# Kernel optimization log

Hardware: AMD Instinct MI355X
Metric: run time of the kernel (lower is better)

The kernel has to match this reference:

```python
import jax, jax.numpy as jnp
import numpy as np
from jax import lax

N_NODES = 64; N_GROUPS = 16; GROUP_SIZE = 4
B = 256; L = 64; CNN_C = 32; GH = 128; DH = 128; OUT = 64
E1 = 262144; E2 = 32768
GROUP_NODES = jnp.arange(N_NODES).reshape(N_GROUPS, GROUP_SIZE)

PARAM_SHAPES = [
    ('conv_w3', (N_NODES, CNN_C, 3)), ('conv_b3', (N_NODES, CNN_C)),
    ('conv_w5', (N_NODES, CNN_C, 5)), ('conv_b5', (N_NODES, CNN_C)),
    ('conv_w7', (N_NODES, CNN_C, 7)), ('conv_b7', (N_NODES, CNN_C)),
    ('tconv_w3', (N_NODES, CNN_C, 3)), ('tconv_b3', (N_NODES, CNN_C)),
    ('tconv_w5', (N_NODES, CNN_C, 5)), ('tconv_b5', (N_NODES, CNN_C)),
    ('tconv_w7', (N_NODES, CNN_C, 7)), ('tconv_b7', (N_NODES, CNN_C)),
    ('ff_w', (N_NODES, 6 * CNN_C, GH)), ('ff_b', (N_NODES, GH)),
    ('lower_w', (GH, GH)), ('lower_b', (GH,)),
    ('upper_w', (GH, GH)), ('upper_b', (GH,)),
    ('agg_w', (N_GROUPS, GROUP_SIZE * GH, GH)), ('agg_b', (N_GROUPS, GH)),
    ('disc_w', (N_GROUPS, 2 * GH, DH)), ('disc_b', (N_GROUPS, DH)),
    ('fc_w', (N_GROUPS * DH, OUT)), ('fc_b', (OUT,)),
]


def setup_inputs() -> dict:
    key = jax.random.key(0)
    ks = jax.random.split(key, 6 + len(PARAM_SHAPES))
    d = {
        'x1': jax.random.normal(ks[0], (B * N_NODES, 4, L), jnp.float32),
        'x2': jax.random.normal(ks[1], (B * N_NODES, 4, L), jnp.float32),
        'edge_index1': jax.random.randint(ks[2], (2, E1), 0, B * N_NODES),
        'edge_index2': jax.random.randint(ks[3], (2, E1), 0, B * N_NODES),
        'group_edge_index1': jax.random.randint(ks[4], (2, E2), 0, B * N_GROUPS),
        'group_edge_index2': jax.random.randint(ks[5], (2, E2), 0, B * N_GROUPS),
    }
    for i, (name, shape) in enumerate(PARAM_SHAPES):
        d[name] = jax.random.normal(ks[6 + i], shape, jnp.float32) * 0.05
    return d


def _grouped_conv_max(x, w, b, pad):
    # x: [B, N, Lx] (one input channel per node), w: [N, C, k], b: [N, C]
    N, C, k = w.shape
    y = lax.conv_general_dilated(x, w.reshape(N * C, 1, k), (1,), [(pad, pad)],
                                 feature_group_count=N,
                                 dimension_numbers=('NCH', 'OIH', 'NCH'))
    y = y + b.reshape(1, N * C, 1)
    return y.max(axis=2).reshape(x.shape[0], N, C)  # max over time per channel


def _gcn(x, edge_index, W, bias):
    # PyG GCNConv: add self loops, symmetric D^-1/2 (A+I) D^-1/2 normalization
    n = x.shape[0]
    loops = jnp.arange(n)
    src = jnp.concatenate([edge_index[0], loops])
    dst = jnp.concatenate([edge_index[1], loops])
    deg = jax.ops.segment_sum(jnp.ones(src.shape[0], x.dtype), dst, n)
    dinv = jnp.where(deg > 0, lax.rsqrt(deg), 0.0)
    h = x @ W
    msg = h[src] * (dinv[src] * dinv[dst])[:, None]
    return jax.ops.segment_sum(msg, dst, n) + bias


def reference(x1, x2, edge_index1, edge_index2, group_edge_index1, group_edge_index2,
              conv_w3, conv_b3, conv_w5, conv_b5, conv_w7, conv_b7,
              tconv_w3, tconv_b3, tconv_w5, tconv_b5, tconv_w7, tconv_b7,
              ff_w, ff_b, lower_w, lower_b, upper_w, upper_b,
              agg_w, agg_b, disc_w, disc_b, fc_w, fc_b):
    def encode(x, ei, gei):
        xr = x.reshape(B, N_NODES, 4, L)  # row = b*N_NODES + n -> x[n::N] == xr[:, n]
        feats = jnp.concatenate([
            _grouped_conv_max(xr[:, :, 0, :], conv_w3, conv_b3, 1),
            _grouped_conv_max(xr[:, :, 0, :], conv_w5, conv_b5, 2),
            _grouped_conv_max(xr[:, :, 0, :], conv_w7, conv_b7, 3),
            _grouped_conv_max(xr[:, :, 1, :-2], tconv_w3, tconv_b3, 1),
            _grouped_conv_max(xr[:, :, 2, :-4], tconv_w5, tconv_b5, 2),
            _grouped_conv_max(xr[:, :, 3, :-6], tconv_w7, tconv_b7, 3),
        ], axis=2)  # [B, N, 6C]
        feats = jax.nn.relu(feats)
        h = jax.nn.relu(jnp.einsum('bnf,nfh->bnh', feats, ff_w) + ff_b)  # per-node Linear
        h = _gcn(h.reshape(B * N_NODES, GH), ei, lower_w, lower_b)
        hg = h.reshape(B, N_NODES, GH)[:, GROUP_NODES]  # [B, G, S, GH]
        hg = hg.reshape(B, N_GROUPS, GROUP_SIZE * GH)
        hg = jnp.einsum('bgf,gfh->bgh', hg, agg_w) + agg_b  # per-group aggregate Linear
        hg = _gcn(hg.reshape(B * N_GROUPS, GH), gei, upper_w, upper_b)
        return jax.nn.relu(hg).reshape(B, N_GROUPS, GH)

    h1 = encode(x1, edge_index1, group_edge_index1)
    h2 = encode(x2, edge_index2, group_edge_index2)
    d = jnp.concatenate([h1, h2], axis=2)  # [B, G, 2*GH]
    d = jax.nn.relu(jnp.einsum('bgf,gfd->bgd', d, disc_w) + disc_b)  # per-group disc fc
    return d.reshape(B, N_GROUPS * DH) @ fc_w + fc_b  # [B, OUT]
```

## Files before the change

### kernel.cpp

```cpp
#include <hip/hip_runtime.h>
#include <hip/hip_bf16.h>

namespace {

constexpr int Bn      = 256;
constexpr int NNODES  = 64;
constexpr int NGROUPS = 16;
constexpr int L       = 64;
constexpr int C       = 32;
constexpr int GH      = 128;
constexpr int E1      = 262144;
constexpr int E2      = 32768;
constexpr int NROWS   = Bn * NNODES;
constexpr int GROWS   = Bn * NGROUPS;
constexpr int XROW    = 296;

template<int K, int LX>
__device__ __forceinline__ void convmax2(const float* __restrict__ xin_al,
                                         const float* __restrict__ wpa,
                                         const float* __restrict__ wpb,
                                         float& ma, float& mb)
{
    constexpr int PAD = (K - 1) / 2;
    constexpr int OFF = 3 - PAD;
    float wa[K], wb[K];
    #pragma unroll
    for (int i = 0; i < K; ++i) { wa[i] = wpa[i]; wb[i] = wpb[i]; }
    ma = -3.0e38f; mb = -3.0e38f;
    #pragma unroll
    for (int p0 = 0; p0 < LX; p0 += 16) {
        float xw[24];
        #pragma unroll
        for (int q = 0; q < 6; ++q) {
            const float4 v = *(const float4*)(xin_al + p0 + q * 4);
            xw[q * 4 + 0] = v.x; xw[q * 4 + 1] = v.y;
            xw[q * 4 + 2] = v.z; xw[q * 4 + 3] = v.w;
        }
        #pragma unroll
        for (int p = 0; p < 16; p += 2) {
            if (p0 + p + 1 < LX) {
                float sa0 = 0.f, sb0 = 0.f, sa1 = 0.f, sb1 = 0.f;
                #pragma unroll
                for (int i = 0; i < K; ++i) {
                    const float xv0 = xw[p + OFF + i];
                    const float xv1 = xw[p + 1 + OFF + i];
                    sa0 = fmaf(wa[i], xv0, sa0);
                    sb0 = fmaf(wb[i], xv0, sb0);
                    sa1 = fmaf(wa[i], xv1, sa1);
                    sb1 = fmaf(wb[i], xv1, sb1);
                }
                ma = fmaxf(fmaxf(sa0, sa1), ma);
                mb = fmaxf(fmaxf(sb0, sb1), mb);
            }
        }
    }
}

__device__ __forceinline__ void conv6_ch0(
    const float* __restrict__ xin_al,
    const float* __restrict__ w3a, const float* __restrict__ w3b,
    const float* __restrict__ w5a, const float* __restrict__ w5b,
    const float* __restrict__ w7a, const float* __restrict__ w7b,
    float& m3a, float& m3b, float& m5a, float& m5b, float& m7a, float& m7b)
{
    float a3[3], b3[3], a5[5], b5[5], a7[7], b7[7];
    #pragma unroll
    for (int i = 0; i < 3; ++i) { a3[i] = w3a[i]; b3[i] = w3b[i]; }
    #pragma unroll
    for (int i = 0; i < 5; ++i) { a5[i] = w5a[i]; b5[i] = w5b[i]; }
    #pragma unroll
    for (int i = 0; i < 7; ++i) { a7[i] = w7a[i]; b7[i] = w7b[i]; }
    m3a = m3b = m5a = m5b = m7a = m7b = -3.0e38f;
    #pragma unroll
    for (int p0 = 0; p0 < 64; p0 += 16) {
        float xw[24];
        #pragma unroll
        for (int q = 0; q < 6; ++q) {
            const float4 v = *(const float4*)(xin_al + p0 + q * 4);
            xw[q * 4 + 0] = v.x; xw[q * 4 + 1] = v.y;
            xw[q * 4 + 2] = v.z; xw[q * 4 + 3] = v.w;
        }
        #pragma unroll
        for (int p = 0; p < 16; p += 2) {
            float s3a0 = 0.f, s3b0 = 0.f, s3a1 = 0.f, s3b1 = 0.f;
            #pragma unroll
            for (int i = 0; i < 3; ++i) {
                const float xv0 = xw[p + 2 + i], xv1 = xw[p + 3 + i];
                s3a0 = fmaf(a3[i], xv0, s3a0); s3b0 = fmaf(b3[i], xv0, s3b0);
                s3a1 = fmaf(a3[i], xv1, s3a1); s3b1 = fmaf(b3[i], xv1, s3b1);
            }
            m3a = fmaxf(fmaxf(s3a0, s3a1), m3a);
            m3b = fmaxf(fmaxf(s3b0, s3b1), m3b);
            float s5a0 = 0.f, s5b0 = 0.f, s5a1 = 0.f, s5b1 = 0.f;
            #pragma unroll
            for (int i = 0; i < 5; ++i) {
                const float xv0 = xw[p + 1 + i], xv1 = xw[p + 2 + i];
                s5a0 = fmaf(a5[i], xv0, s5a0); s5b0 = fmaf(b5[i], xv0, s5b0);
                s5a1 = fmaf(a5[i], xv1, s5a1); s5b1 = fmaf(b5[i], xv1, s5b1);
            }
            m5a = fmaxf(fmaxf(s5a0, s5a1), m5a);
            m5b = fmaxf(fmaxf(s5b0, s5b1), m5b);
            float s7a0 = 0.f, s7b0 = 0.f, s7a1 = 0.f, s7b1 = 0.f;
            #pragma unroll
            for (int i = 0; i < 7; ++i) {
                const float xv0 = xw[p + 0 + i], xv1 = xw[p + 1 + i];
                s7a0 = fmaf(a7[i], xv0, s7a0); s7b0 = fmaf(b7[i], xv0, s7b0);
                s7a1 = fmaf(a7[i], xv1, s7a1); s7b1 = fmaf(b7[i], xv1, s7b1);
            }
            m7a = fmaxf(fmaxf(s7a0, s7a1), m7a);
            m7b = fmaxf(fmaxf(s7b0, s7b1), m7b);
        }
    }
}

__global__ __launch_bounds__(256) void k_conv_feats(
    const float* __restrict__ x1, const float* __restrict__ x2,
    const float* __restrict__ w3,  const float* __restrict__ b3,
    const float* __restrict__ w5,  const float* __restrict__ b5,
    const float* __restrict__ w7,  const float* __restrict__ b7,
    const float* __restrict__ tw3, const float* __restrict__ tb3,
    const float* __restrict__ tw5, const float* __restrict__ tb5,
    const float* __restrict__ tw7, const float* __restrict__ tb7,
    float* __restrict__ feats)
{
    __shared__ float xs[16 * XROW];
    const int t = threadIdx.x;
    const int eb = blockIdx.x >> 10;
    const float* __restrict__ x = eb ? x2 : x1;
    const int row0 = (blockIdx.x & 1023) * 16;
    for (int idx = t; idx < 16 * 4 * 72; idx += 256) {
        const int r   = idx / 288;
        const int rem = idx - r * 288;
        const int c   = rem / 72;
        const int j   = rem - c * 72;
        const int l   = j - 3;
        float v = 0.f;
        if (l >= 0 && l < 64 - 2 * c)
            v = x[(size_t)(row0 + r) * 256 + c * 64 + l];
        xs[r * XROW + c * 72 + j] = v;
    }
    __syncthreads();

    const int rr  = t >> 4;
    const int cp  = t & 15;
    const int ch0 = cp * 2;
    const int row = row0 + rr;
    const int n   = row & (NNODES - 1);
    const int wc0 = n * C + ch0;
    const int wc1 = wc0 + 1;
    const float* xb0 = &xs[rr * XROW + 0 * 72];
    const float* xb1 = &xs[rr * XROW + 1 * 72];
    const float* xb2 = &xs[rr * XROW + 2 * 72];
    const float* xb3 = &xs[rr * XROW + 3 * 72];

    float* o = feats + (size_t)(eb * NROWS + row) * 192 + ch0;

    float m3a, m3b, m5a, m5b, m7a, m7b;
    conv6_ch0(xb0, w3 + wc0 * 3, w3 + wc1 * 3, w5 + wc0 * 5, w5 + wc1 * 5,
              w7 + wc0 * 7, w7 + wc1 * 7, m3a, m3b, m5a, m5b, m7a, m7b);
    *(float2*)(o + 0 * 32) = make_float2(fmaxf(m3a + b3[wc0], 0.f), fmaxf(m3b + b3[wc1], 0.f));
    *(float2*)(o + 1 * 32) = make_float2(fmaxf(m5a + b5[wc0], 0.f), fmaxf(m5b + b5[wc1], 0.f));
    *(float2*)(o + 2 * 32) = make_float2(fmaxf(m7a + b7[wc0], 0.f), fmaxf(m7b + b7[wc1], 0.f));

    float ma, mb;
    convmax2<3, 62>(xb1, tw3 + wc0 * 3, tw3 + wc1 * 3, ma, mb);
    *(float2*)(o + 3 * 32) = make_float2(fmaxf(ma + tb3[wc0], 0.f), fmaxf(mb + tb3[wc1], 0.f));
    convmax2<5, 60>(xb2, tw5 + wc0 * 5, tw5 + wc1 * 5, ma, mb);
    *(float2*)(o + 4 * 32) = make_float2(fmaxf(ma + tb5[wc0], 0.f), fmaxf(mb + tb5[wc1], 0.f));
    convmax2<7, 58>(xb3, tw7 + wc0 * 7, tw7 + wc1 * 7, ma, mb);
    *(float2*)(o + 5 * 32) = make_float2(fmaxf(ma + tb7[wc0], 0.f), fmaxf(mb + tb7[wc1], 0.f));
}

__global__ __launch_bounds__(256) void k_ff_lower(
    const float* __restrict__ feats, const float* __restrict__ ffw,
    const float* __restrict__ ffb, const float* __restrict__ lw,
    float* __restrict__ hw)
{
    const int nb = blockIdx.x >> 6;
    const int n  = blockIdx.x & 63;
    const int t  = threadIdx.x;
    const int o  = t & 127;
    const int rh = t >> 7;
    __shared__ float fs[16 * 192];
    __shared__ float h0s[16 * 128];
    {
        float4* d4 = (float4*)fs;
        for (int i = t; i < 16 * 48; i += 256) {
            const int r = i / 48, c4 = i - r * 48;
            d4[i] = *(const float4*)(feats + ((size_t)(nb * 16 + r) * 64 + n) * 192 + c4 * 4);
        }
    }
    __syncthreads();
    {
        const float* w = ffw + (size_t)n * 192 * 128 + o;
        float acc[8];
        #pragma unroll
        for (int r = 0; r < 8; ++r) acc[r] = 0.f;
        #pragma unroll 2
        for (int f = 0; f < 192; f += 4) {
            const float w0 = w[(f + 0) * 128];
            const float w1 = w[(f + 1) * 128];
            const float w2 = w[(f + 2) * 128];
            const float w3_ = w[(f + 3) * 128];
            #pragma unroll
            for (int r = 0; r < 8; ++r) {
                const float4 xv = *(const float4*)(fs + (rh * 8 + r) * 192 + f);
                acc[r] = fmaf(xv.x, w0, acc[r]);
                acc[r] = fmaf(xv.y, w1, acc[r]);
                acc[r] = fmaf(xv.z, w2, acc[r]);
                acc[r] = fmaf(xv.w, w3_, acc[r]);
            }
        }
        const float bias = ffb[n * 128 + o];
        #pragma unroll
        for (int r = 0; r < 8; ++r)
            h0s[(rh * 8 + r) * 128 + o] = fmaxf(acc[r] + bias, 0.f);
    }
    __syncthreads();
    {
        const float* w = lw + o;
        float acc[8];
        #pragma unroll
        for (int r = 0; r < 8; ++r) acc[r] = 0.f;
        #pragma unroll 2
        for (int f = 0; f < 128; f += 4) {
            const float w0 = w[(f + 0) * 128];
            const float w1 = w[(f + 1) * 128];
            const float w2 = w[(f + 2) * 128];
            const float w3_ = w[(f + 3) * 128];
            #pragma unroll
            for (int r = 0; r < 8; ++r) {
                const float4 xv = *(const float4*)(h0s + (rh * 8 + r) * 128 + f);
                acc[r] = fmaf(xv.x, w0, acc[r]);
                acc[r] = fmaf(xv.y, w1, acc[r]);
                acc[r] = fmaf(xv.z, w2, acc[r]);
                acc[r] = fmaf(xv.w, w3_, acc[r]);
            }
        }
        #pragma unroll
        for (int r = 0; r < 8; ++r) {
            const int row = nb * 16 + rh * 8 + r;
            hw[((size_t)row * 64 + n) * 128 + o] = acc[r];
        }
    }
}

__global__ __launch_bounds__(256) void k_gemm128(
    const float* __restrict__ X, const float* __restrict__ W,
    float* __restrict__ Y)
{
    const int r0 = blockIdx.x * 16;
    const int t  = threadIdx.x;
    const int o  = t & 127;
    const int rh = t >> 7;
    __shared__ float xs[16 * 128];
    {
        float4* d4 = (float4*)xs;
        const float4* s4 = (const float4*)(X + (size_t)r0 * 128);
        for (int i = t; i < 512; i += 256) d4[i] = s4[i];
    }
    __syncthreads();
    const float* w = W + o;
    float acc[8];
    #pragma unroll
    for (int r = 0; r < 8; ++r) acc[r] = 0.f;
    #pragma unroll 2
    for (int f = 0; f < 128; f += 4) {
        const float w0 = w[(f + 0) * 128];
        const float w1 = w[(f + 1) * 128];
        const float w2 = w[(f + 2) * 128];
        const float w3_ = w[(f + 3) * 128];
        #pragma unroll
        for (int r = 0; r < 8; ++r) {
            const float4 xv = *(const float4*)(xs + (rh * 8 + r) * 128 + f);
            acc[r] = fmaf(xv.x, w0, acc[r]);
            acc[r] = fmaf(xv.y, w1, acc[r]);
            acc[r] = fmaf(xv.z, w2, acc[r]);
            acc[r] = fmaf(xv.w, w3_, acc[r]);
        }
    }
    #pragma unroll
    for (int r = 0; r < 8; ++r)
        Y[(size_t)(r0 + rh * 8 + r) * 128 + o] = acc[r];
}

__global__ void k_zero_i(int* __restrict__ p, int n) {
    const int i = blockIdx.x * blockDim.x + threadIdx.x;
    if (i < n) p[i] = 0;
}
__global__ void k_hist_all(const int* __restrict__ ei0, const int* __restrict__ ei1,
                           const int* __restrict__ gei0, const int* __restrict__ gei1,
                           int* __restrict__ cnt1, int* __restrict__ cnt2)
{
    const int gid = blockIdx.x * blockDim.x + threadIdx.x;
    if (gid < 2 * E1) {
        const int eb = gid >= E1;
        const int le = gid - (eb ? E1 : 0);
        const int* ei = eb ? ei1 : ei0;
        atomicAdd(&cnt1[(eb ? NROWS : 0) + ei[E1 + le]], 1);
    } else {
        const int g2 = gid - 2 * E1;
        const int eb = g2 >= E2;
        const int le = g2 - (eb ? E2 : 0);
        const int* ei = eb ? gei1 : gei0;
        atomicAdd(&cnt2[(eb ? GROWS : 0) + ei[E2 + le]], 1);
    }
}
__global__ __launch_bounds__(256) void k_scan_bsum_all(
    const int* __restrict__ cnt1, const int* __restrict__ cnt2,
    int* __restrict__ bsum1, int* __restrict__ bsum2)
{
    const int blk = blockIdx.x, t = threadIdx.x;
    const int* cnt; int* bsum; int lblk;
    if (blk < 32) { cnt = cnt1; bsum = bsum1; lblk = blk; }
    else          { cnt = cnt2; bsum = bsum2; lblk = blk - 32; }
    const int4 v = ((const int4*)cnt)[lblk * 256 + t];
    int s = v.x + v.y + v.z + v.w;
    #pragma unroll
    for (int off = 32; off > 0; off >>= 1) s += __shfl_down(s, off);
    __shared__ int wsum[4];
    if ((t & 63) == 0) wsum[t >> 6] = s;
    __syncthreads();
    if (t == 0) bsum[lblk] = wsum[0] + wsum[1] + wsum[2] + wsum[3];
}
__global__ __launch_bounds__(256) void k_scan_final_all(
    const int* __restrict__ cnt1, const int* __restrict__ bsum1,
    int* __restrict__ offs1, int* __restrict__ cur1, float* __restrict__ dinv1,
    const int* __restrict__ cnt2, const int* __restrict__ bsum2,
    int* __restrict__ offs2, int* __restrict__ cur2, float* __restrict__ dinv2)
{
    const int blk = blockIdx.x, t = threadIdx.x;
    const int* cnt; const int* bsum; int* offs; int* cur; float* dinv;
    int n, nb, lblk;
    if (blk < 32) { cnt = cnt1; bsum = bsum1; offs = offs1; cur = cur1; dinv = dinv1;
                    n = 2 * NROWS; nb = 32; lblk = blk; }
    else          { cnt = cnt2; bsum = bsum2; offs = offs2; cur = cur2; dinv = dinv2;
                    n = 2 * GROWS; nb = 8; lblk = blk - 32; }
    int base = 0;
    for (int i = 0; i < lblk; ++i) base += bsum[i];
    const int4 v = ((const int4*)cnt)[lblk * 256 + t];
    const int s = v.x + v.y + v.z + v.w;
    int sc = s;
    #pragma unroll
    for (int off = 1; off < 64; off <<= 1) {
        const int u = __shfl_up(sc, off);
        if ((t & 63) >= off) sc += u;
    }
    __shared__ int wsum[4];
    if ((t & 63) == 63) wsum[t >> 6] = sc;
    __syncthreads();
    int wbase = 0;
    for (int wv = 0; wv < (t >> 6); ++wv) wbase += wsum[wv];
    int o0 = base + wbase + sc - s;
    const int gi = lblk * 1024 + t * 4;
    offs[gi + 0] = o0; cur[gi + 0] = o0; dinv[gi + 0] = rsqrtf(1.f + (float)v.x); o0 += v.x;
    offs[gi + 1] = o0; cur[gi + 1] = o0; dinv[gi + 1] = rsqrtf(1.f + (float)v.y); o0 += v.y;
    offs[gi + 2] = o0; cur[gi + 2] = o0; dinv[gi + 2] = rsqrtf(1.f + (float)v.z); o0 += v.z;
    offs[gi + 3] = o0; cur[gi + 3] = o0; dinv[gi + 3] = rsqrtf(1.f + (float)v.w); o0 += v.w;
    if (lblk == nb - 1 && t == 255) offs[n] = o0;
}
__global__ void k_fill_all(const int* __restrict__ ei0, const int* __restrict__ ei1,
                           const int* __restrict__ gei0, const int* __restrict__ gei1,
                           int* __restrict__ cur1, int* __restrict__ esrc1,
                           int* __restrict__ cur2, int* __restrict__ esrc2)
{
    const int gid = blockIdx.x * blockDim.x + threadIdx.x;
    if (gid < 2 * E1) {
        const int eb = gid >= E1;
        const int le = gid - (eb ? E1 : 0);
        const int* ei = eb ? ei1 : ei0;
        const int s = ei[le];
        const int d = ei[E1 + le];
        const int pos = atomicAdd(&cur1[(eb ? NROWS : 0) + d], 1);
        esrc1[pos] = s;
    } else {
        const int g2 = gid - 2 * E1;
        const int eb = g2 >= E2;
        const int le = g2 - (eb ? E2 : 0);
        const int* ei = eb ? gei1 : gei0;
        const int s = ei[le];
        const int d = ei[E2 + le];
        const int pos = atomicAdd(&cur2[(eb ? GROWS : 0) + d], 1);
        esrc2[pos] = s;
    }
}

__global__ __launch_bounds__(128) void k_gcn_gather(
    const int* __restrict__ offs, const int* __restrict__ esrc,
    const float* __restrict__ hw, const float* __restrict__ dinv,
    const float* __restrict__ bias, float* __restrict__ out, int n)
{
    const int d = blockIdx.x;
    const int t = threadIdx.x;
    const int sbase = (d >= n) ? n : 0;
    const int e0 = offs[d], e1 = offs[d + 1];
    const float dd = dinv[d];
    float a0 = hw[(size_t)d * 128 + t] * dd;
    float a1 = 0.f, a2 = 0.f, a3 = 0.f;
    int j = e0;
    for (; j + 3 < e1; j += 4) {
        const int s0 = sbase + esrc[j],     s1 = sbase + esrc[j + 1];
        const int s2 = sbase + esrc[j + 2], s3 = sbase + esrc[j + 3];
        a0 = fmaf(hw[(size_t)s0 * 128 + t], dinv[s0], a0);
        a1 = fmaf(hw[(size_t)s1 * 128 + t], dinv[s1], a1);
        a2 = fmaf(hw[(size_t)s2 * 128 + t], dinv[s2], a2);
        a3 = fmaf(hw[(size_t)s3 * 128 + t], dinv[s3], a3);
    }
    for (; j < e1; ++j) {
        const int s = sbase + esrc[j];
        a0 = fmaf(hw[(size_t)s * 128 + t], dinv[s], a0);
    }
    const float acc = (a0 + a1) + (a2 + a3);
    out[(size_t)d * 128 + t] = fmaf(acc, dd, bias[t]);
}

__global__ __launch_bounds__(256) void k_agg(
    const float* __restrict__ h, const float* __restrict__ aggw,
    const float* __restrict__ aggb, float* __restrict__ hg)
{
    const int bt = blockIdx.x >> 4;
    const int g  = blockIdx.x & 15;
    const int t  = threadIdx.x;
    const int o  = t & 127;
    const int kk = t >> 7;
    __shared__ float fs[4 * 512];
    __shared__ float red[2][4][128];
    {
        const int b0 = bt * 4;
        float4* dst = (float4*)fs;
        for (int i = t; i < 4 * 128; i += 256) {
            const int r = i >> 7;
            const int q = i & 127;
            dst[i] = *(const float4*)(h + ((size_t)(b0 + r) * 64 + g * 4) * 128 + q * 4);
        }
    }
    __syncthreads();
    const float* w = aggw + (size_t)g * 512 * 128 + (size_t)kk * 256 * 128 + o;
    float a0 = 0.f, a1 = 0.f, a2 = 0.f, a3 = 0.f;
    const float* x0 = fs + 0 * 512 + kk * 256;
    const float* x1 = fs + 1 * 512 + kk * 256;
    const float* x2 = fs + 2 * 512 + kk * 256;
    const float* x3 = fs + 3 * 512 + kk * 256;
    #pragma unroll 8
    for (int f = 0; f < 256; ++f) {
        const float wv = w[f * 128];
        a0 = fmaf(x0[f], wv, a0);
        a1 = fmaf(x1[f], wv, a1);
        a2 = fmaf(x2[f], wv, a2);
        a3 = fmaf(x3[f], wv, a3);
    }
    red[kk][0][o] = a0; red[kk][1][o] = a1; red[kk][2][o] = a2; red[kk][3][o] = a3;
    __syncthreads();
    if (t < 128) {
        const float bias = aggb[g * 128 + t];
        #pragma unroll
        for (int r = 0; r < 4; ++r) {
            const int b = bt * 4 + r;
            hg[((size_t)b * 16 + g) * 128 + t] = red[0][r][t] + red[1][r][t] + bias;
        }
    }
}

__global__ __launch_bounds__(256) void k_gdisc(
    const int* __restrict__ offs, const int* __restrict__ esrc,
    const float* __restrict__ hgw, const float* __restrict__ dinv,
    const float* __restrict__ ub,
    const float* __restrict__ dw, const float* __restrict__ db,
    float* __restrict__ dd)
{
    const int bt = blockIdx.x >> 4;
    const int g  = blockIdx.x & 15;
    const int t  = threadIdx.x;
    const int o  = t & 127;
    const int hf = t >> 7;
    __shared__ float fsA[2][8][128];
    __shared__ float fs[4][256];
    __shared__ float red[2][4][128];

    for (int r = 0; r < 8; ++r) {
        const int bi = r >> 1, eb = r & 1;
        const int sbase = eb ? GROWS : 0;
        const int drow = sbase + (bt * 4 + bi) * 16 + g;
        const int e0 = offs[drow], e1 = offs[drow + 1];
        float acc  = (hf == 0) ? hgw[(size_t)drow * 128 + o] * dinv[drow] : 0.f;
        float acc2 = 0.f;
        int jj = e0 + hf;
        for (; jj + 2 < e1; jj += 4) {
            const int s0 = sbase + esrc[jj];
            const int s1 = sbase + esrc[jj + 2];
            acc  = fmaf(hgw[(size_t)s0 * 128 + o], dinv[s0], acc);
            acc2 = fmaf(hgw[(size_t)s1 * 128 + o], dinv[s1], acc2);
        }
        for (; jj < e1; jj += 2) {
            const int s = sbase + esrc[jj];
            acc = fmaf(hgw[(size_t)s * 128 + o], dinv[s], acc);
        }
        fsA[hf][r][o] = acc + acc2;
    }
    __syncthreads();
    for (int idx = t; idx < 1024; idx += 256) {
        const int r = idx >> 7, oc = idx & 127;
        const int bi = r >> 1, eb = r & 1;
        const int sbase = eb ? GROWS : 0;
        const int drow = sbase + (bt * 4 + bi) * 16 + g;
        fs[bi][eb * 128 + oc] =
            fmaxf(fmaf(fsA[0][r][oc] + fsA[1][r][oc], dinv[drow], ub[oc]), 0.f);
    }
    __syncthreads();
    {
        const float* w = dw + (size_t)g * 256 * 128 + (size_t)hf * 128 * 128 + o;
        float a0 = 0.f, a1 = 0.f, a2 = 0.f, a3 = 0.f;
        const float* x0 = &fs[0][hf * 128];
        const float* x1 = &fs[1][hf * 128];
        const float* x2 = &fs[2][hf * 128];
        const float* x3 = &fs[3][hf * 128];
        #pragma unroll 8
        for (int f = 0; f < 128; ++f) {
            const float wv = w[f * 128];
            a0 = fmaf(x0[f], wv, a0);
            a1 = fmaf(x1[f], wv, a1);
            a2 = fmaf(x2[f], wv, a2);
            a3 = fmaf(x3[f], wv, a3);
        }
        red[hf][0][o] = a0; red[hf][1][o] = a1; red[hf][2][o] = a2; red[hf][3][o] = a3;
    }
    __syncthreads();
    if (t < 128) {
        const float bias = db[g * 128 + t];
        #pragma unroll
        for (int r = 0; r < 4; ++r) {
            const int b = bt * 4 + r;
            dd[(size_t)b * 2048 + g * 128 + t] =
                fmaxf(red[0][r][t] + red[1][r][t] + bias, 0.f);
        }
    }
}

__global__ __launch_bounds__(256) void k_fc(
    const float* __restrict__ dd, const float* __restrict__ fcw,
    const float* __restrict__ fcb, float* __restrict__ out)
{
    const int b = blockIdx.x;
    const int t = threadIdx.x;
    const int o = t & 63;
    const int k = t >> 6;
    __shared__ float ds[2048];
    __shared__ float red[4][64];
    for (int i = t; i < 2048; i += 256) ds[i] = dd[(size_t)b * 2048 + i];
    __syncthreads();
    const float* w  = fcw + (k * 512) * 64 + o;
    const float* xr = ds + k * 512;
    float a0 = 0.f, a1 = 0.f, a2 = 0.f, a3 = 0.f;
    #pragma unroll 4
    for (int f = 0; f < 512; f += 4) {
        a0 = fmaf(xr[f + 0], w[(f + 0) * 64], a0);
        a1 = fmaf(xr[f + 1], w[(f + 1) * 64], a1);
        a2 = fmaf(xr[f + 2], w[(f + 2) * 64], a2);
        a3 = fmaf(xr[f + 3], w[(f + 3) * 64], a3);
    }
    red[k][o] = (a0 + a1) + (a2 + a3);
    __syncthreads();
    if (t < 64)
        out[(size_t)b * 64 + t] = ((red[0][t] + red[1][t]) + (red[2][t] + red[3][t])) + fcb[t];
}

}

extern "C" void kernel_launch(void* const* d_in, const int* in_sizes, int n_in,
                              void* d_out, int out_size, void* d_ws, size_t ws_size,
                              hipStream_t stream)
{
    const float* x1 = (const float*)d_in[0];
    const float* x2 = (const float*)d_in[1];
    const int* ei0  = (const int*)d_in[2];
    const int* ei1  = (const int*)d_in[3];
    const int* gei0 = (const int*)d_in[4];
    const int* gei1 = (const int*)d_in[5];
    const float* conv_w3 = (const float*)d_in[6];
    const float* conv_b3 = (const float*)d_in[7];
    const float* conv_w5 = (const float*)d_in[8];
    const float* conv_b5 = (const float*)d_in[9];
    const float* conv_w7 = (const float*)d_in[10];
    const float* conv_b7 = (const float*)d_in[11];
    const float* tconv_w3 = (const float*)d_in[12];
    const float* tconv_b3 = (const float*)d_in[13];
    const float* tconv_w5 = (const float*)d_in[14];
    const float* tconv_b5 = (const float*)d_in[15];
    const float* tconv_w7 = (const float*)d_in[16];
    const float* tconv_b7 = (const float*)d_in[17];
    const float* ff_w    = (const float*)d_in[18];
    const float* ff_b    = (const float*)d_in[19];
    const float* lower_w = (const float*)d_in[20];
    const float* lower_b = (const float*)d_in[21];
    const float* upper_w = (const float*)d_in[22];
    const float* upper_b = (const float*)d_in[23];
    const float* agg_w   = (const float*)d_in[24];
    const float* agg_b   = (const float*)d_in[25];
    const float* disc_w  = (const float*)d_in[26];
    const float* disc_b  = (const float*)d_in[27];
    const float* fc_w    = (const float*)d_in[28];
    const float* fc_b    = (const float*)d_in[29];

    float* ws = (float*)d_ws;
    float* f_feats = ws;
    float* f_hw    = ws + 10485760;
    float* f_gout  = ws + 14680064;
    float* f_hg    = ws + 18874368;
    float* f_hgw   = ws + 19922944;
    float* f_dd    = ws + 22020096;
    float* f_dinv1 = ws + 22544384;
    float* f_dinv2 = ws + 22577152;
    int* ip    = (int*)(ws + 22585344);
    int* cnt1  = ip;
    int* cnt2  = cnt1 + 2 * NROWS;
    int* offs1 = cnt2 + 2 * GROWS;
    int* cur1  = offs1 + 2 * NROWS + 1;
    int* esrc1 = cur1 + 2 * NROWS;
    int* offs2 = esrc1 + 2 * E1;
    int* cur2  = offs2 + 2 * GROWS + 1;
    int* esrc2 = cur2 + 2 * GROWS;
    int* bsum1 = esrc2 + 2 * E2;
    int* bsum2 = bsum1 + 32;

    k_zero_i<<<(2 * NROWS + 2 * GROWS) / 256, 256, 0, stream>>>(cnt1, 2 * NROWS + 2 * GROWS);
    k_hist_all<<<(2 * E1 + 2 * E2) / 256, 256, 0, stream>>>(ei0, ei1, gei0, gei1, cnt1, cnt2);
    k_scan_bsum_all<<<40, 256, 0, stream>>>(cnt1, cnt2, bsum1, bsum2);
    k_scan_final_all<<<40, 256, 0, stream>>>(cnt1, bsum1, offs1, cur1, f_dinv1,
                                             cnt2, bsum2, offs2, cur2, f_dinv2);
    k_fill_all<<<(2 * E1 + 2 * E2) / 256, 256, 0, stream>>>(ei0, ei1, gei0, gei1,
                                                            cur1, esrc1, cur2, esrc2);

    k_conv_feats<<<2 * NROWS / 16, 256, 0, stream>>>(x1, x2,
        conv_w3, conv_b3, conv_w5, conv_b5, conv_w7, conv_b7,
        tconv_w3, tconv_b3, tconv_w5, tconv_b5, tconv_w7, tconv_b7, f_feats);
    k_ff_lower<<<2048, 256, 0, stream>>>(f_feats, ff_w, ff_b, lower_w, f_hw);
    k_gcn_gather<<<2 * NROWS, 128, 0, stream>>>(offs1, esrc1, f_hw, f_dinv1,
                                                lower_b, f_gout, NROWS);
    k_agg<<<2 * (Bn / 4) * 16, 256, 0, stream>>>(f_gout, agg_w, agg_b, f_hg);
    k_gemm128<<<2 * GROWS / 16, 256, 0, stream>>>(f_hg, upper_w, f_hgw);
    k_gdisc<<<1024, 256, 0, stream>>>(offs2, esrc2, f_hgw, f_dinv2, upper_b,
                                      disc_w, disc_b, f_dd);
    k_fc<<<Bn, 256, 0, stream>>>(f_dd, fc_w, fc_b, (float*)d_out);
}
```

Baseline: 287.5 us.

## Fuse CSR build into conv/ff kernels and merge agg with upper GEMM

Folds the edge histogram into the conv kernel and the CSR fill into the ff_lower kernel as extra blocks, so graph preprocessing runs alongside the dense compute and needs fewer launches. It also fuses the per-group aggregate linear with the upper-GCN 128x128 GEMM, keeping the intermediate group features in shared memory instead of writing and re-reading them. The cost is larger, heterogeneous grids where atomic-heavy blocks compete with compute blocks, and the conv kernel carries a shared-memory allocation that the histogram blocks never use.

```diff
diff --git a/kernel.cpp b/kernel.cpp
--- a/kernel.cpp
+++ b/kernel.cpp
@@ -113,7 +113,7 @@
     }
 }
 
-__global__ __launch_bounds__(256) void k_conv_feats(
+__global__ __launch_bounds__(256) void k_conv_hist(
     const float* __restrict__ x1, const float* __restrict__ x2,
     const float* __restrict__ w3,  const float* __restrict__ b3,
     const float* __restrict__ w5,  const float* __restrict__ b5,
@@ -121,10 +121,29 @@
     const float* __restrict__ tw3, const float* __restrict__ tb3,
     const float* __restrict__ tw5, const float* __restrict__ tb5,
     const float* __restrict__ tw7, const float* __restrict__ tb7,
-    float* __restrict__ feats)
+    float* __restrict__ feats,
+    const int* __restrict__ ei0, const int* __restrict__ ei1,
+    const int* __restrict__ gei0, const int* __restrict__ gei1,
+    int* __restrict__ cnt1, int* __restrict__ cnt2)
 {
     __shared__ float xs[16 * XROW];
     const int t = threadIdx.x;
+    if (blockIdx.x >= 2048) {
+        const int gid = (blockIdx.x - 2048) * 256 + t;
+        if (gid < 2 * E1) {
+            const int eb = gid >= E1;
+            const int le = gid - (eb ? E1 : 0);
+            const int* ei = eb ? ei1 : ei0;
+            atomicAdd(&cnt1[(eb ? NROWS : 0) + ei[E1 + le]], 1);
+        } else {
+            const int g2 = gid - 2 * E1;
+            const int eb = g2 >= E2;
+            const int le = g2 - (eb ? E2 : 0);
+            const int* ei = eb ? gei1 : gei0;
+            atomicAdd(&cnt2[(eb ? GROWS : 0) + ei[E2 + le]], 1);
+        }
+        return;
+    }
     const int eb = blockIdx.x >> 10;
     const float* __restrict__ x = eb ? x2 : x1;
     const int row0 = (blockIdx.x & 1023) * 16;
@@ -171,18 +190,44 @@
     *(float2*)(o + 5 * 32) = make_float2(fmaxf(ma + tb7[wc0], 0.f), fmaxf(mb + tb7[wc1], 0.f));
 }
 
-__global__ __launch_bounds__(256) void k_ff_lower(
+__global__ __launch_bounds__(256) void k_ff_lower_fill(
     const float* __restrict__ feats, const float* __restrict__ ffw,
     const float* __restrict__ ffb, const float* __restrict__ lw,
-    float* __restrict__ hw)
-{
+    float* __restrict__ hw,
+    const int* __restrict__ ei0, const int* __restrict__ ei1,
+    const int* __restrict__ gei0, const int* __restrict__ gei1,
+    int* __restrict__ cur1, int* __restrict__ esrc1,
+    int* __restrict__ cur2, int* __restrict__ esrc2)
+{
+    __shared__ float fs[16 * 192];
+    __shared__ float h0s[16 * 128];
+    const int t = threadIdx.x;
+    if (blockIdx.x >= 2048) {
+        const int gid = (blockIdx.x - 2048) * 256 + t;
+        if (gid < 2 * E1) {
+            const int eb = gid >= E1;
+            const int le = gid - (eb ? E1 : 0);
+            const int* ei = eb ? ei1 : ei0;
+            const int s = ei[le];
+            const int d = ei[E1 + le];
+            const int pos = atomicAdd(&cur1[(eb ? NROWS : 0) + d], 1);
+            esrc1[pos] = s;
+        } else {
+            const int g2 = gid - 2 * E1;
+            const int eb = g2 >= E2;
+            const int le = g2 - (eb ? E2 : 0);
+            const int* ei = eb ? gei1 : gei0;
+            const int s = ei[le];
+            const int d = ei[E2 + le];
+            const int pos = atomicAdd(&cur2[(eb ? GROWS : 0) + d], 1);
+            esrc2[pos] = s;
+        }
+        return;
+    }
     const int nb = blockIdx.x >> 6;
     const int n  = blockIdx.x & 63;
-    const int t  = threadIdx.x;
     const int o  = t & 127;
     const int rh = t >> 7;
-    __shared__ float fs[16 * 192];
-    __shared__ float h0s[16 * 128];
     {
         float4* d4 = (float4*)fs;
         for (int i = t; i < 16 * 48; i += 256) {
@@ -245,66 +290,9 @@
     }
 }
 
-__global__ __launch_bounds__(256) void k_gemm128(
-    const float* __restrict__ X, const float* __restrict__ W,
-    float* __restrict__ Y)
-{
-    const int r0 = blockIdx.x * 16;
-    const int t  = threadIdx.x;
-    const int o  = t & 127;
-    const int rh = t >> 7;
-    __shared__ float xs[16 * 128];
-    {
-        float4* d4 = (float4*)xs;
-        const float4* s4 = (const float4*)(X + (size_t)r0 * 128);
-        for (int i = t; i < 512; i += 256) d4[i] = s4[i];
-    }
-    __syncthreads();
-    const float* w = W + o;
-    float acc[8];
-    #pragma unroll
-    for (int r = 0; r < 8; ++r) acc[r] = 0.f;
-    #pragma unroll 2
-    for (int f = 0; f < 128; f += 4) {
-        const float w0 = w[(f + 0) * 128];
-        const float w1 = w[(f + 1) * 128];
-        const float w2 = w[(f + 2) * 128];
-        const float w3_ = w[(f + 3) * 128];
-        #pragma unroll
-        for (int r = 0; r < 8; ++r) {
-            const float4 xv = *(const float4*)(xs + (rh * 8 + r) * 128 + f);
-            acc[r] = fmaf(xv.x, w0, acc[r]);
-            acc[r] = fmaf(xv.y, w1, acc[r]);
-            acc[r] = fmaf(xv.z, w2, acc[r]);
-            acc[r] = fmaf(xv.w, w3_, acc[r]);
-        }
-    }
-    #pragma unroll
-    for (int r = 0; r < 8; ++r)
-        Y[(size_t)(r0 + rh * 8 + r) * 128 + o] = acc[r];
-}
-
 __global__ void k_zero_i(int* __restrict__ p, int n) {
     const int i = blockIdx.x * blockDim.x + threadIdx.x;
     if (i < n) p[i] = 0;
-}
-__global__ void k_hist_all(const int* __restrict__ ei0, const int* __restrict__ ei1,
-                           const int* __restrict__ gei0, const int* __restrict__ gei1,
-                           int* __restrict__ cnt1, int* __restrict__ cnt2)
-{
-    const int gid = blockIdx.x * blockDim.x + threadIdx.x;
-    if (gid < 2 * E1) {
-        const int eb = gid >= E1;
-        const int le = gid - (eb ? E1 : 0);
-        const int* ei = eb ? ei1 : ei0;
-        atomicAdd(&cnt1[(eb ? NROWS : 0) + ei[E1 + le]], 1);
-    } else {
-        const int g2 = gid - 2 * E1;
-        const int eb = g2 >= E2;
-        const int le = g2 - (eb ? E2 : 0);
-        const int* ei = eb ? gei1 : gei0;
-        atomicAdd(&cnt2[(eb ? GROWS : 0) + ei[E2 + le]], 1);
-    }
 }
 __global__ __launch_bounds__(256) void k_scan_bsum_all(
     const int* __restrict__ cnt1, const int* __restrict__ cnt2,
@@ -358,31 +346,6 @@
     offs[gi + 2] = o0; cur[gi + 2] = o0; dinv[gi + 2] = rsqrtf(1.f + (float)v.z); o0 += v.z;
     offs[gi + 3] = o0; cur[gi + 3] = o0; dinv[gi + 3] = rsqrtf(1.f + (float)v.w); o0 += v.w;
     if (lblk == nb - 1 && t == 255) offs[n] = o0;
-}
-__global__ void k_fill_all(const int* __restrict__ ei0, const int* __restrict__ ei1,
-                           const int* __restrict__ gei0, const int* __restrict__ gei1,
-                           int* __restrict__ cur1, int* __restrict__ esrc1,
-                           int* __restrict__ cur2, int* __restrict__ esrc2)
-{
-    const int gid = blockIdx.x * blockDim.x + threadIdx.x;
-    if (gid < 2 * E1) {
-        const int eb = gid >= E1;
-        const int le = gid - (eb ? E1 : 0);
-        const int* ei = eb ? ei1 : ei0;
-        const int s = ei[le];
-        const int d = ei[E1 + le];
-        const int pos = atomicAdd(&cur1[(eb ? NROWS : 0) + d], 1);
-        esrc1[pos] = s;
-    } else {
-        const int g2 = gid - 2 * E1;
-        const int eb = g2 >= E2;
-        const int le = g2 - (eb ? E2 : 0);
-        const int* ei = eb ? gei1 : gei0;
-        const int s = ei[le];
-        const int d = ei[E2 + le];
-        const int pos = atomicAdd(&cur2[(eb ? GROWS : 0) + d], 1);
-        esrc2[pos] = s;
-    }
 }
 
 __global__ __launch_bounds__(128) void k_gcn_gather(
@@ -414,17 +377,19 @@
     out[(size_t)d * 128 + t] = fmaf(acc, dd, bias[t]);
 }
 
-__global__ __launch_bounds__(256) void k_agg(
+__global__ __launch_bounds__(256) void k_aggup(
     const float* __restrict__ h, const float* __restrict__ aggw,
-    const float* __restrict__ aggb, float* __restrict__ hg)
+    const float* __restrict__ aggb, const float* __restrict__ uw,
+    float* __restrict__ hgw)
 {
     const int bt = blockIdx.x >> 4;
     const int g  = blockIdx.x & 15;
     const int t  = threadIdx.x;
     const int o  = t & 127;
-    const int kk = t >> 7;
+    const int hf = t >> 7;
     __shared__ float fs[4 * 512];
     __shared__ float red[2][4][128];
+    __shared__ float hgs[4][128];
     {
         const int b0 = bt * 4;
         float4* dst = (float4*)fs;
@@ -435,29 +400,50 @@
         }
     }
     __syncthreads();
-    const float* w = aggw + (size_t)g * 512 * 128 + (size_t)kk * 256 * 128 + o;
-    float a0 = 0.f, a1 = 0.f, a2 = 0.f, a3 = 0.f;
-    const float* x0 = fs + 0 * 512 + kk * 256;
-    const float* x1 = fs + 1 * 512 + kk * 256;
-    const float* x2 = fs + 2 * 512 + kk * 256;
-    const float* x3 = fs + 3 * 512 + kk * 256;
-    #pragma unroll 8
-    for (int f = 0; f < 256; ++f) {
-        const float wv = w[f * 128];
-        a0 = fmaf(x0[f], wv, a0);
-        a1 = fmaf(x1[f], wv, a1);
-        a2 = fmaf(x2[f], wv, a2);
-        a3 = fmaf(x3[f], wv, a3);
-    }
-    red[kk][0][o] = a0; red[kk][1][o] = a1; red[kk][2][o] = a2; red[kk][3][o] = a3;
+    {
+        const float* w = aggw + (size_t)g * 512 * 128 + (size_t)hf * 256 * 128 + o;
+        float a0 = 0.f, a1 = 0.f, a2 = 0.f, a3 = 0.f;
+        const float* x0 = fs + 0 * 512 + hf * 256;
+        const float* x1 = fs + 1 * 512 + hf * 256;
+        const float* x2 = fs + 2 * 512 + hf * 256;
+        const float* x3 = fs + 3 * 512 + hf * 256;
+        #pragma unroll 8
+        for (int f = 0; f < 256; ++f) {
+            const float wv = w[f * 128];
+            a0 = fmaf(x0[f], wv, a0);
+            a1 = fmaf(x1[f], wv, a1);
+            a2 = fmaf(x2[f], wv, a2);
+            a3 = fmaf(x3[f], wv, a3);
+        }
+        red[hf][0][o] = a0; red[hf][1][o] = a1; red[hf][2][o] = a2; red[hf][3][o] = a3;
+    }
     __syncthreads();
     if (t < 128) {
         const float bias = aggb[g * 128 + t];
         #pragma unroll
-        for (int r = 0; r < 4; ++r) {
-            const int b = bt * 4 + r;
-            hg[((size_t)b * 16 + g) * 128 + t] = red[0][r][t] + red[1][r][t] + bias;
-        }
+        for (int r = 0; r < 4; ++r)
+            hgs[r][t] = red[0][r][t] + red[1][r][t] + bias;
+    }
+    __syncthreads();
+    {
+        const float* w = uw + o;
+        float a0 = 0.f, a1 = 0.f;
+        #pragma unroll 2
+        for (int f = 0; f < 128; f += 4) {
+            const float w0 = w[(f + 0) * 128];
+            const float w1 = w[(f + 1) * 128];
+            const float w2 = w[(f + 2) * 128];
+            const float w3_ = w[(f + 3) * 128];
+            const float4 xv0 = *(const float4*)(&hgs[hf * 2 + 0][f]);
+            const float4 xv1 = *(const float4*)(&hgs[hf * 2 + 1][f]);
+            a0 = fmaf(xv0.x, w0, a0); a0 = fmaf(xv0.y, w1, a0);
+            a0 = fmaf(xv0.z, w2, a0); a0 = fmaf(xv0.w, w3_, a0);
+            a1 = fmaf(xv1.x, w0, a1); a1 = fmaf(xv1.y, w1, a1);
+            a1 = fmaf(xv1.z, w2, a1); a1 = fmaf(xv1.w, w3_, a1);
+        }
+        const int r0g = (bt * 4 + hf * 2) * 16 + g;
+        hgw[(size_t)r0g * 128 + o] = a0;
+        hgw[(size_t)(r0g + 16) * 128 + o] = a1;
     }
 }
 
@@ -605,7 +591,6 @@
     float* f_feats = ws;
     float* f_hw    = ws + 10485760;
     float* f_gout  = ws + 14680064;
-    float* f_hg    = ws + 18874368;
     float* f_hgw   = ws + 19922944;
     float* f_dd    = ws + 22020096;
     float* f_dinv1 = ws + 22544384;
@@ -623,21 +608,19 @@
     int* bsum2 = bsum1 + 32;
 
     k_zero_i<<<(2 * NROWS + 2 * GROWS) / 256, 256, 0, stream>>>(cnt1, 2 * NROWS + 2 * GROWS);
-    k_hist_all<<<(2 * E1 + 2 * E2) / 256, 256, 0, stream>>>(ei0, ei1, gei0, gei1, cnt1, cnt2);
+    k_conv_hist<<<2048 + (2 * E1 + 2 * E2) / 256, 256, 0, stream>>>(x1, x2,
+        conv_w3, conv_b3, conv_w5, conv_b5, conv_w7, conv_b7,
+        tconv_w3, tconv_b3, tconv_w5, tconv_b5, tconv_w7, tconv_b7, f_feats,
+        ei0, ei1, gei0, gei1, cnt1, cnt2);
     k_scan_bsum_all<<<40, 256, 0, stream>>>(cnt1, cnt2, bsum1, bsum2);
     k_scan_final_all<<<40, 256, 0, stream>>>(cnt1, bsum1, offs1, cur1, f_dinv1,
                                              cnt2, bsum2, offs2, cur2, f_dinv2);
-    k_fill_all<<<(2 * E1 + 2 * E2) / 256, 256, 0, stream>>>(ei0, ei1, gei0, gei1,
-                                                            cur1, esrc1, cur2, esrc2);
-
-    k_conv_feats<<<2 * NROWS / 16, 256, 0, stream>>>(x1, x2,
-        conv_w3, conv_b3, conv_w5, conv_b5, conv_w7, conv_b7,
-        tconv_w3, tconv_b3, tconv_w5, tconv_b5, tconv_w7, tconv_b7, f_feats);
-    k_ff_lower<<<2048, 256, 0, stream>>>(f_feats, ff_w, ff_b, lower_w, f_hw);
+    k_ff_lower_fill<<<2048 + (2 * E1 + 2 * E2) / 256, 256, 0, stream>>>(
+        f_feats, ff_w, ff_b, lower_w, f_hw,
+        ei0, ei1, gei0, gei1, cur1, esrc1, cur2, esrc2);
     k_gcn_gather<<<2 * NROWS, 128, 0, stream>>>(offs1, esrc1, f_hw, f_dinv1,
                                                 lower_b, f_gout, NROWS);
-    k_agg<<<2 * (Bn / 4) * 16, 256, 0, stream>>>(f_gout, agg_w, agg_b, f_hg);
-    k_gemm128<<<2 * GROWS / 16, 256, 0, stream>>>(f_hg, upper_w, f_hgw);
+    k_aggup<<<2048, 256, 0, stream>>>(f_gout, agg_w, agg_b, upper_w, f_hgw);
     k_gdisc<<<1024, 256, 0, stream>>>(offs2, esrc2, f_hgw, f_dinv2, upper_b,
                                       disc_w, disc_b, f_dd);
     k_fc<<<Bn, 256, 0, stream>>>(f_dd, fc_w, fc_b, (float*)d_out);
```

After: 255.3 us. 1.13x faster.
